# Optimization experiments

Measured on AMD Instinct MI355X. Metric: run time of the kernel, lower is better.

The kernel has to match this reference:

```python
import jax, jax.numpy as jnp
import numpy as np
from jax import lax

B, CIN, COUT, H, W = 4, 32, 64, 192, 192
K = 3  # kernel size
RED = 16  # SE reduction
EPS = 1e-5


def _conv2d_same(x, w, b):
    y = lax.conv_general_dilated(x, w, (1, 1), 'SAME',
                                 dimension_numbers=('NCHW', 'OIHW', 'NCHW'))
    return y + b[None, :, None, None]


def _bilinear_gather(x, py, px):
    # x: [B,C,H,W]; py/px: [B,KK,H,W] absolute sample coords -> [B,C,KK,H,W]
    Bb, C, Hh, Ww = x.shape
    KK = py.shape[1]
    y0 = jnp.floor(py); x0 = jnp.floor(px)
    wy = py - y0; wx = px - x0
    x_flat = x.reshape(Bb, C, Hh * Ww)

    def corner(yi, xi, wgt):
        valid = (yi >= 0) & (yi < Hh) & (xi >= 0) & (xi < Ww)
        yc = jnp.clip(yi, 0, Hh - 1).astype(jnp.int32)
        xc = jnp.clip(xi, 0, Ww - 1).astype(jnp.int32)
        idx = (yc * Ww + xc).reshape(Bb, 1, KK * Hh * Ww)
        g = jnp.take_along_axis(x_flat, idx, axis=2).reshape(Bb, C, KK, Hh, Ww)
        w_eff = (wgt * valid.astype(x.dtype))[:, None]  # [B,1,KK,H,W]
        return g * w_eff

    out = (corner(y0, x0, (1 - wy) * (1 - wx))
           + corner(y0, x0 + 1, (1 - wy) * wx)
           + corner(y0 + 1, x0, wy * (1 - wx))
           + corner(y0 + 1, x0 + 1, wy * wx))
    return out  # [B,C,KK,H,W]


def _deform_conv(x, offsets, w, b):
    # torchvision DeformConv2d, stride 1, pad 1, dilation 1, 1 offset group.
    Bb, C, Hh, Ww = x.shape
    off = offsets.reshape(Bb, K * K, 2, Hh, Ww)
    dy, dx = off[:, :, 0], off[:, :, 1]  # [B,KK,H,W]
    ky, kx = jnp.meshgrid(jnp.arange(K) - 1, jnp.arange(K) - 1, indexing='ij')
    hg, wg = jnp.meshgrid(jnp.arange(Hh), jnp.arange(Ww), indexing='ij')
    py = hg[None, None] + ky.reshape(-1)[None, :, None, None] + dy
    px = wg[None, None] + kx.reshape(-1)[None, :, None, None] + dx
    sampled = _bilinear_gather(x, py, px)  # [B,CIN,KK,H,W]
    y = jnp.einsum('bckhw,ock->bohw', sampled, w.reshape(w.shape[0], C, K * K))
    return y + b[None, :, None, None]


def _forward(x, w_off, b_off, w_def, b_def, bn_gamma, bn_beta,
             fc1_w, fc1_b, fc2_w, fc2_b):
    offsets = _conv2d_same(x, w_off, b_off)
    y = _deform_conv(x, offsets, w_def, b_def)
    # BatchNorm2d (training-mode batch statistics)
    mean = jnp.mean(y, axis=(0, 2, 3), keepdims=True)
    var = jnp.var(y, axis=(0, 2, 3), keepdims=True)
    y = (y - mean) * lax.rsqrt(var + EPS)
    y = y * bn_gamma[None, :, None, None] + bn_beta[None, :, None, None]
    # SE layer
    s = jnp.mean(y, axis=(2, 3))  # [B,C]
    s = jax.nn.relu(s @ fc1_w.T + fc1_b)
    s = jax.nn.sigmoid(s @ fc2_w.T + fc2_b)
    y = y * s[:, :, None, None]
    y = jax.nn.relu(y)
    # MaxPool 2x2 stride 2
    y = lax.reduce_window(y, -jnp.inf, lax.max, (1, 1, 2, 2), (1, 1, 2, 2), 'VALID')
    return y


def setup_inputs() -> dict:
    key = jax.random.key(0)
    ks = jax.random.split(key, 12)
    rn = lambda k, s, sc=1.0: (jax.random.normal(k, s, dtype=jnp.float32) * sc)
    return {
        'x': rn(ks[0], (B, CIN, H, W)),
        'w_off': rn(ks[1], (2 * K * K, CIN, K, K), 0.02),
        'b_off': jnp.zeros((2 * K * K,), jnp.float32),
        'w_def': rn(ks[2], (COUT, CIN, K, K), 0.05),
        'b_def': rn(ks[3], (COUT,), 0.05),
        'bn_gamma': jnp.ones((COUT,), jnp.float32),
        'bn_beta': jnp.zeros((COUT,), jnp.float32),
        'fc1_w': rn(ks[4], (COUT // RED, COUT), 0.1),
        'fc1_b': jnp.zeros((COUT // RED,), jnp.float32),
        'fc2_w': rn(ks[5], (COUT, COUT // RED), 0.1),
        'fc2_b': jnp.zeros((COUT,), jnp.float32),
    }


def reference(x, w_off, b_off, w_def, b_def, bn_gamma, bn_beta,
              fc1_w, fc1_b, fc2_w, fc2_b):
    return _forward(x, w_off, b_off, w_def, b_def, bn_gamma, bn_beta,
                    fc1_w, fc1_b, fc2_w, fc2_b)
```

## Files before the change

### kernel.cpp

```cpp
#include <hip/hip_runtime.h>
#include <math.h>

#define B_    4
#define CIN_  32
#define COUT_ 64
#define H_    192
#define W_    192
#define HW_   (H_ * W_)
#define NPIX_ (B_ * HW_)
#define EPS_  1e-5f

static __device__ __forceinline__ int swz1152(int blk) {
    return ((blk & 7) * 144) + (blk >> 3);
}
static __device__ __forceinline__ int swz2304(int blk) {
    return ((blk & 7) * 288) + (blk >> 3);
}

struct Cr { int o00, o01, o10, o11; float w00, w01, w10, w11; };

__global__ __launch_bounds__(256) void k_pre(
    const float* __restrict__ x, const float* __restrict__ w_def,
    const float* __restrict__ w_off, float* __restrict__ xt,
    float* __restrict__ wt_def, float* __restrict__ wt_off,
    float* __restrict__ stats)
{
    if (blockIdx.x < NPIX_ / 256) {
        const int pid = blockIdx.x * 256 + threadIdx.x;
        const int b   = pid / HW_;
        const int rem = pid - b * HW_;
        const float* xb = x + (size_t)b * CIN_ * HW_ + rem;
        float4 v[8];
#pragma unroll
        for (int j = 0; j < 8; ++j) {
            v[j].x = xb[(j * 4 + 0) * HW_];
            v[j].y = xb[(j * 4 + 1) * HW_];
            v[j].z = xb[(j * 4 + 2) * HW_];
            v[j].w = xb[(j * 4 + 3) * HW_];
        }
        float4* dst = (float4*)(xt + (size_t)pid * 32);
#pragma unroll
        for (int j = 0; j < 8; ++j) dst[j] = v[j];
    } else {
        const int i = (blockIdx.x - NPIX_ / 256) * 256 + threadIdx.x;
        if (i < 18432) {
            const int o  = i & 63;
            const int c  = (i >> 6) & 31;
            const int kk = i >> 11;
            wt_def[i] = w_def[(o * 32 + c) * 9 + kk];
        } else if (i < 18432 + 5760) {
            const int e  = i - 18432;
            const int c  = e & 31;
            const int t  = e >> 5;
            const int o  = t % 20;
            const int kk = t / 20;
            wt_off[e] = (o < 18) ? w_off[(o * 32 + c) * 9 + kk] : 0.f;
        } else if (i < 18432 + 5760 + 512) {
            stats[i - 18432 - 5760] = 0.f;
        }
    }
}

__global__ __launch_bounds__(256, 6) void k_conv_off(
    const float* __restrict__ xt, const float* __restrict__ wt,
    const float* __restrict__ b_off, float* __restrict__ offs)
{
    __shared__ float4 tile[8][198];
    const int tid = threadIdx.x;
    const int px  = tid & 63;
    const int og  = __builtin_amdgcn_readfirstlane(tid >> 6);

    const int blk  = swz2304(blockIdx.x);
    const int base = blk * 64;
    const int b    = base / HW_;
    const int rem0 = base - b * HW_;
    const int h0   = rem0 / W_;
    const int w0   = rem0 - h0 * W_;

    const float* xb = xt + (size_t)b * HW_ * 32;
    for (int i = tid; i < 1584; i += 256) {
        const int j   = i & 7;
        const int rec = i >> 3;
        const int r   = rec / 66;
        const int cc  = rec - r * 66;
        const int hc  = min(max(h0 + r - 1, 0), H_ - 1);
        const int wc  = min(max(w0 + cc - 1, 0), W_ - 1);
        tile[j][rec] = *(const float4*)(xb + (hc * W_ + wc) * 32 + j * 4);
    }
    __syncthreads();

    const bool rv0 = (h0 - 1 >= 0), rv2 = (h0 + 1 < H_);
    float acc[5] = {0.f, 0.f, 0.f, 0.f, 0.f};

#pragma unroll 1
    for (int kk = 0; kk < 9; ++kk) {
        const int ky = kk / 3, kx = kk % 3;
        const bool rok = (ky == 0) ? rv0 : ((ky == 2) ? rv2 : true);
        const int wcol = w0 + px + kx - 1;
        const float g = (rok && wcol >= 0 && wcol < W_) ? 1.f : 0.f;
        const int rec = ky * 66 + px + kx;

        float4 v[8];
#pragma unroll
        for (int j = 0; j < 8; ++j) {
            v[j] = tile[j][rec];
            v[j].x *= g; v[j].y *= g; v[j].z *= g; v[j].w *= g;
        }
        const float* wk = wt + (kk * 20 + og * 5) * 32;
#pragma unroll
        for (int oo = 0; oo < 5; ++oo) {
            const float4* wr = (const float4*)(wk + oo * 32);
            float s = acc[oo];
#pragma unroll
            for (int j = 0; j < 8; ++j) {
                const float4 wv = wr[j];
                s += v[j].x * wv.x + v[j].y * wv.y
                   + v[j].z * wv.z + v[j].w * wv.w;
            }
            acc[oo] = s;
        }
    }

    const int rem = rem0 + px;
#pragma unroll
    for (int oo = 0; oo < 5; ++oo) {
        const int o = og * 5 + oo;
        if (o < 18)
            offs[(b * 18 + o) * HW_ + rem] = acc[oo] + b_off[o];
    }
}

__global__ __launch_bounds__(512, 6) void k_deform(
    const float* __restrict__ xt, const float* __restrict__ offs,
    const float* __restrict__ wt, const float* __restrict__ b_def,
    float* __restrict__ y, float* __restrict__ sum_bc,
    float* __restrict__ sumsq_bc)
{
    __shared__ float vlds[32 * 128];
    const int tid  = threadIdx.x;
    const int px   = tid & 127;
    const int grp  = __builtin_amdgcn_readfirstlane(tid >> 7);
    const int lane = tid & 63;
    const int pid  = swz1152(blockIdx.x) * 128 + px;
    const int b    = pid / HW_;
    const int rem  = pid - b * HW_;
    const int h    = rem / W_;
    const int w    = rem - h * W_;
    const float* xg = xt + (size_t)b * HW_ * 32 + grp * 8;
    const float* ob = offs + b * 18 * HW_ + rem;

    float acc[16];
#pragma unroll
    for (int q = 0; q < 16; ++q) acc[q] = 0.f;

    auto mk = [&](int kk, float dy, float dx) -> Cr {
        const float py = (float)(h + kk / 3 - 1) + dy;
        const float qx = (float)(w + kk % 3 - 1) + dx;
        const float y0f = floorf(py), x0f = floorf(qx);
        const float wy = py - y0f, wx = qx - x0f;
        const int iy0 = (int)y0f, ix0 = (int)x0f;
        const int iy1 = iy0 + 1,  ix1 = ix0 + 1;
        const float vy0 = (iy0 >= 0 && iy0 < H_) ? 1.f : 0.f;
        const float vy1 = (iy1 >= 0 && iy1 < H_) ? 1.f : 0.f;
        const float vx0 = (ix0 >= 0 && ix0 < W_) ? 1.f : 0.f;
        const float vx1 = (ix1 >= 0 && ix1 < W_) ? 1.f : 0.f;
        Cr c;
        c.w00 = (1.f - wy) * (1.f - wx) * vy0 * vx0;
        c.w01 = (1.f - wy) * wx * vy0 * vx1;
        c.w10 = wy * (1.f - wx) * vy1 * vx0;
        c.w11 = wy * wx * vy1 * vx1;
        const int cy0 = min(max(iy0, 0), H_ - 1), cy1 = min(max(iy1, 0), H_ - 1);
        const int cx0 = min(max(ix0, 0), W_ - 1), cx1 = min(max(ix1, 0), W_ - 1);
        c.o00 = (cy0 * W_ + cx0) * 32; c.o01 = (cy0 * W_ + cx1) * 32;
        c.o10 = (cy1 * W_ + cx0) * 32; c.o11 = (cy1 * W_ + cx1) * 32;
        return c;
    };

    float dy = ob[0], dx = ob[HW_];
    Cr cur = mk(0, dy, dx);
    float4 A0 = *(const float4*)(xg + cur.o00), A1 = *(const float4*)(xg + cur.o00 + 4);
    float4 B0 = *(const float4*)(xg + cur.o01), B1 = *(const float4*)(xg + cur.o01 + 4);
    float4 C0 = *(const float4*)(xg + cur.o10), C1 = *(const float4*)(xg + cur.o10 + 4);
    float4 D0 = *(const float4*)(xg + cur.o11), D1 = *(const float4*)(xg + cur.o11 + 4);
    float ndy = ob[2 * HW_], ndx = ob[3 * HW_];

#pragma unroll 1
    for (int kk = 0; kk < 9; ++kk) {
        __syncthreads();
        float v[8];
        v[0] = cur.w00 * A0.x + cur.w01 * B0.x + cur.w10 * C0.x + cur.w11 * D0.x;
        v[1] = cur.w00 * A0.y + cur.w01 * B0.y + cur.w10 * C0.y + cur.w11 * D0.y;
        v[2] = cur.w00 * A0.z + cur.w01 * B0.z + cur.w10 * C0.z + cur.w11 * D0.z;
        v[3] = cur.w00 * A0.w + cur.w01 * B0.w + cur.w10 * C0.w + cur.w11 * D0.w;
        v[4] = cur.w00 * A1.x + cur.w01 * B1.x + cur.w10 * C1.x + cur.w11 * D1.x;
        v[5] = cur.w00 * A1.y + cur.w01 * B1.y + cur.w10 * C1.y + cur.w11 * D1.y;
        v[6] = cur.w00 * A1.z + cur.w01 * B1.z + cur.w10 * C1.z + cur.w11 * D1.z;
        v[7] = cur.w00 * A1.w + cur.w01 * B1.w + cur.w10 * C1.w + cur.w11 * D1.w;
#pragma unroll
        for (int j = 0; j < 8; ++j) vlds[(grp * 8 + j) * 128 + px] = v[j];

        if (kk < 8) {
            cur = mk(kk + 1, ndy, ndx);
            A0 = *(const float4*)(xg + cur.o00); A1 = *(const float4*)(xg + cur.o00 + 4);
            B0 = *(const float4*)(xg + cur.o01); B1 = *(const float4*)(xg + cur.o01 + 4);
            C0 = *(const float4*)(xg + cur.o10); C1 = *(const float4*)(xg + cur.o10 + 4);
            D0 = *(const float4*)(xg + cur.o11); D1 = *(const float4*)(xg + cur.o11 + 4);
            if (kk < 7) {
                ndy = ob[(2 * kk + 4) * HW_];
                ndx = ob[(2 * kk + 5) * HW_];
            }
        }
        __syncthreads();

        const float* wk = wt + (kk << 11) + (grp << 4);
#pragma unroll 8
        for (int c = 0; c < 32; ++c) {
            const float vv = vlds[c * 128 + px];
            const float4* wr = (const float4*)(wk + (c << 6));
            const float4 w0 = wr[0], w1 = wr[1], w2 = wr[2], w3 = wr[3];
            acc[ 0] += vv * w0.x; acc[ 1] += vv * w0.y;
            acc[ 2] += vv * w0.z; acc[ 3] += vv * w0.w;
            acc[ 4] += vv * w1.x; acc[ 5] += vv * w1.y;
            acc[ 6] += vv * w1.z; acc[ 7] += vv * w1.w;
            acc[ 8] += vv * w2.x; acc[ 9] += vv * w2.y;
            acc[10] += vv * w2.z; acc[11] += vv * w2.w;
            acc[12] += vv * w3.x; acc[13] += vv * w3.y;
            acc[14] += vv * w3.z; acc[15] += vv * w3.w;
        }
    }

    float* yp = y + ((size_t)b * COUT_ + grp * 16) * HW_ + rem;
#pragma unroll
    for (int q = 0; q < 16; ++q) {
        acc[q] += b_def[grp * 16 + q];
        yp[q * HW_] = acc[q];
    }

    float ls = 0.f, lq = 0.f;
#pragma unroll
    for (int o = 0; o < 16; ++o) {
        float t = acc[o];
        float u = t * t;
#pragma unroll
        for (int s = 32; s; s >>= 1) {
            t += __shfl_xor(t, s, 64);
            u += __shfl_xor(u, s, 64);
        }
        if (lane == o) { ls = t; lq = u; }
    }
    if (lane < 16) {
        atomicAdd(&sum_bc[b * 64 + grp * 16 + lane], ls);
        atomicAdd(&sumsq_bc[b * 64 + grp * 16 + lane], lq);
    }
}

__global__ __launch_bounds__(256) void k_finish(
    const float* __restrict__ y,
    const float* __restrict__ sum_bc, const float* __restrict__ sumsq_bc,
    const float* __restrict__ gamma, const float* __restrict__ beta,
    const float* __restrict__ fc1_w, const float* __restrict__ fc1_b,
    const float* __restrict__ fc2_w, const float* __restrict__ fc2_b,
    float* __restrict__ out)
{
    __shared__ float sal[256], sbb[256], sin_[256];
    const int tid = threadIdx.x;
    {
        const int b = tid >> 6, c = tid & 63;
        float ch_s = 0.f, ch_q = 0.f;
#pragma unroll
        for (int bb = 0; bb < 4; ++bb) {
            ch_s += sum_bc[bb * 64 + c];
            ch_q += sumsq_bc[bb * 64 + c];
        }
        const float invN = 1.f / (float)(B_ * HW_);
        const float mean = ch_s * invN;
        const float var  = ch_q * invN - mean * mean;
        const float a    = gamma[c] * rsqrtf(var + EPS_);
        const float bi   = beta[c] - mean * a;
        sin_[tid] = a * (sum_bc[tid] * (1.f / (float)HW_)) + bi;
        __syncthreads();
        float hv[4];
#pragma unroll
        for (int j = 0; j < 4; ++j) {
            float hs = fc1_b[j];
            for (int cc = 0; cc < 64; ++cc)
                hs += sin_[b * 64 + cc] * fc1_w[j * 64 + cc];
            hv[j] = fmaxf(hs, 0.f);
        }
        float o = fc2_b[c];
#pragma unroll
        for (int j = 0; j < 4; ++j) o += hv[j] * fc2_w[c * 4 + j];
        const float s = 1.f / (1.f + expf(-o));
        sal[tid] = a * s;
        sbb[tid] = bi * s;
    }
    __syncthreads();

    const int t    = blockIdx.x * 256 + tid;
    const int opix = t * 2;
    const int bc   = opix / (96 * 96);
    const int rem  = opix - bc * (96 * 96);
    const int oh   = rem / 96, ow = rem - oh * 96;
    const float al = sal[bc], bb = sbb[bc];
    const float* yp = y + (size_t)bc * HW_ + (2 * oh) * W_ + 2 * ow;
    const float4 r0 = *(const float4*)yp;
    const float4 r1 = *(const float4*)(yp + W_);
    float2 st;
    st.x = fmaxf(fmaxf(fmaxf(fmaf(r0.x, al, bb), fmaf(r0.y, al, bb)),
                       fmaxf(fmaf(r1.x, al, bb), fmaf(r1.y, al, bb))), 0.f);
    st.y = fmaxf(fmaxf(fmaxf(fmaf(r0.z, al, bb), fmaf(r0.w, al, bb)),
                       fmaxf(fmaf(r1.z, al, bb), fmaf(r1.w, al, bb))), 0.f);
    *(float2*)(out + opix) = st;
}

extern "C" void kernel_launch(void* const* d_in, const int* in_sizes, int n_in,
                              void* d_out, int out_size, void* d_ws, size_t ws_size,
                              hipStream_t stream)
{
    const float* x     = (const float*)d_in[0];
    const float* w_off = (const float*)d_in[1];
    const float* b_off = (const float*)d_in[2];
    const float* w_def = (const float*)d_in[3];
    const float* b_def = (const float*)d_in[4];
    const float* gamma = (const float*)d_in[5];
    const float* beta  = (const float*)d_in[6];
    const float* fc1_w = (const float*)d_in[7];
    const float* fc1_b = (const float*)d_in[8];
    const float* fc2_w = (const float*)d_in[9];
    const float* fc2_b = (const float*)d_in[10];
    float* out = (float*)d_out;

    float* ws   = (float*)d_ws;
    float* offs   = ws;
    float* yb     = offs + 2654208;
    float* xt     = yb + 9437184;
    float* wt_def = xt + 4718592;
    float* wt_off = wt_def + 18432;
    float* stats  = wt_off + 5760;
    float* sum_bc   = stats;
    float* sumsq_bc = stats + 256;

    k_pre     <<<dim3(NPIX_ / 256 + 97), dim3(256), 0, stream>>>(
                  x, w_def, w_off, xt, wt_def, wt_off, stats);
    k_conv_off<<<dim3(NPIX_ / 64), dim3(256), 0, stream>>>(xt, wt_off, b_off, offs);
    k_deform  <<<dim3(NPIX_ / 128), dim3(512), 0, stream>>>(xt, offs, wt_def, b_def,
                                                            yb, sum_bc, sumsq_bc);
    k_finish  <<<dim3(B_ * COUT_ * 96 * 96 / 512), dim3(256), 0, stream>>>(
                  yb, sum_bc, sumsq_bc, gamma, beta,
                  fc1_w, fc1_b, fc2_w, fc2_b, out);
}
```

Before: 264.7 us.

## Fuse offset conv into deformable conv kernel with LDS double-buffered sampling

Merges the offset-prediction convolution and the deformable convolution into one kernel. Offsets now stay in shared memory and are never written to or read back from global memory. The block shrinks from 128 to 64 pixels with 4 groups of 16 output channels each. The per-tap sampled values are double-buffered in LDS, so each tap needs one barrier instead of two and the next tap's gathers overlap the current FMA loop. The trade-off is one fewer kernel launch and less offset traffic, against smaller blocks, reuse of the tile buffer, and possible register pressure from holding the prefetched corners across the inner loop.

Measured after the change: 224.6 us. 15.1% less time.

```diff
diff --git a/kernel.cpp b/kernel.cpp
--- a/kernel.cpp
+++ b/kernel.cpp
@@ -10,9 +10,6 @@
 #define NPIX_ (B_ * HW_)
 #define EPS_  1e-5f
 
-static __device__ __forceinline__ int swz1152(int blk) {
-    return ((blk & 7) * 144) + (blk >> 3);
-}
 static __device__ __forceinline__ int swz2304(int blk) {
     return ((blk & 7) * 288) + (blk >> 3);
 }
@@ -61,14 +58,21 @@
     }
 }
 
-__global__ __launch_bounds__(256, 6) void k_conv_off(
-    const float* __restrict__ xt, const float* __restrict__ wt,
-    const float* __restrict__ b_off, float* __restrict__ offs)
+__global__ __launch_bounds__(256, 6) void k_fused(
+    const float* __restrict__ xt, const float* __restrict__ wto,
+    const float* __restrict__ b_off, const float* __restrict__ wtd,
+    const float* __restrict__ b_def, float* __restrict__ y,
+    float* __restrict__ sum_bc, float* __restrict__ sumsq_bc)
 {
-    __shared__ float4 tile[8][198];
-    const int tid = threadIdx.x;
-    const int px  = tid & 63;
-    const int og  = __builtin_amdgcn_readfirstlane(tid >> 6);
+    __shared__ __align__(16) float smem[6336];
+    __shared__ float offlds[20 * 64];
+    float4 (*tile)[198] = (float4(*)[198])smem;
+    float* vbuf = smem;
+
+    const int tid  = threadIdx.x;
+    const int px   = tid & 63;
+    const int og   = __builtin_amdgcn_readfirstlane(tid >> 6);
+    const int lane = tid & 63;
 
     const int blk  = swz2304(blockIdx.x);
     const int base = blk * 64;
@@ -76,8 +80,8 @@
     const int rem0 = base - b * HW_;
     const int h0   = rem0 / W_;
     const int w0   = rem0 - h0 * W_;
-
     const float* xb = xt + (size_t)b * HW_ * 32;
+
     for (int i = tid; i < 1584; i += 256) {
         const int j   = i & 7;
         const int rec = i >> 3;
@@ -89,71 +93,56 @@
     }
     __syncthreads();
 
-    const bool rv0 = (h0 - 1 >= 0), rv2 = (h0 + 1 < H_);
-    float acc[5] = {0.f, 0.f, 0.f, 0.f, 0.f};
-
+    {
+        const bool rv0 = (h0 - 1 >= 0), rv2 = (h0 + 1 < H_);
+        float acc5[5] = {0.f, 0.f, 0.f, 0.f, 0.f};
 #pragma unroll 1
-    for (int kk = 0; kk < 9; ++kk) {
-        const int ky = kk / 3, kx = kk % 3;
-        const bool rok = (ky == 0) ? rv0 : ((ky == 2) ? rv2 : true);
-        const int wcol = w0 + px + kx - 1;
-        const float g = (rok && wcol >= 0 && wcol < W_) ? 1.f : 0.f;
-        const int rec = ky * 66 + px + kx;
-
-        float4 v[8];
-#pragma unroll
-        for (int j = 0; j < 8; ++j) {
-            v[j] = tile[j][rec];
-            v[j].x *= g; v[j].y *= g; v[j].z *= g; v[j].w *= g;
-        }
-        const float* wk = wt + (kk * 20 + og * 5) * 32;
+        for (int kk = 0; kk < 9; ++kk) {
+            const int ky = kk / 3, kx = kk % 3;
+            const bool rok = (ky == 0) ? rv0 : ((ky == 2) ? rv2 : true);
+            const int wcol = w0 + px + kx - 1;
+            const float g = (rok && wcol >= 0 && wcol < W_) ? 1.f : 0.f;
+            const int rec = ky * 66 + px + kx;
+
+            float4 v[8];
+#pragma unroll
+            for (int j = 0; j < 8; ++j) {
+                v[j] = tile[j][rec];
+                v[j].x *= g; v[j].y *= g; v[j].z *= g; v[j].w *= g;
+            }
+            const float* wk = wto + (kk * 20 + og * 5) * 32;
+#pragma unroll
+            for (int oo = 0; oo < 5; ++oo) {
+                const float4* wr = (const float4*)(wk + oo * 32);
+                float s = acc5[oo];
+#pragma unroll
+                for (int j = 0; j < 8; ++j) {
+                    const float4 wv = wr[j];
+                    s += v[j].x * wv.x + v[j].y * wv.y
+                       + v[j].z * wv.z + v[j].w * wv.w;
+                }
+                acc5[oo] = s;
+            }
+        }
 #pragma unroll
         for (int oo = 0; oo < 5; ++oo) {
-            const float4* wr = (const float4*)(wk + oo * 32);
-            float s = acc[oo];
-#pragma unroll
-            for (int j = 0; j < 8; ++j) {
-                const float4 wv = wr[j];
-                s += v[j].x * wv.x + v[j].y * wv.y
-                   + v[j].z * wv.z + v[j].w * wv.w;
-            }
-            acc[oo] = s;
-        }
-    }
-
-    const int rem = rem0 + px;
-#pragma unroll
-    for (int oo = 0; oo < 5; ++oo) {
-        const int o = og * 5 + oo;
-        if (o < 18)
-            offs[(b * 18 + o) * HW_ + rem] = acc[oo] + b_off[o];
-    }
-}
-
-__global__ __launch_bounds__(512, 6) void k_deform(
-    const float* __restrict__ xt, const float* __restrict__ offs,
-    const float* __restrict__ wt, const float* __restrict__ b_def,
-    float* __restrict__ y, float* __restrict__ sum_bc,
-    float* __restrict__ sumsq_bc)
-{
-    __shared__ float vlds[32 * 128];
-    const int tid  = threadIdx.x;
-    const int px   = tid & 127;
-    const int grp  = __builtin_amdgcn_readfirstlane(tid >> 7);
-    const int lane = tid & 63;
-    const int pid  = swz1152(blockIdx.x) * 128 + px;
-    const int b    = pid / HW_;
-    const int rem  = pid - b * HW_;
-    const int h    = rem / W_;
-    const int w    = rem - h * W_;
-    const float* xg = xt + (size_t)b * HW_ * 32 + grp * 8;
-    const float* ob = offs + b * 18 * HW_ + rem;
+            const int o = og * 5 + oo;
+            if (o < 18) offlds[o * 64 + px] = acc5[oo] + b_off[o];
+        }
+    }
+    __syncthreads();
+
+    const int h = h0;
+    const int w = w0 + px;
+    const float* xg = xb + og * 8;
 
     float acc[16];
 #pragma unroll
     for (int q = 0; q < 16; ++q) acc[q] = 0.f;
 
-    auto mk = [&](int kk, float dy, float dx) -> Cr {
+    auto mk = [&](int kk) -> Cr {
+        const float dy = offlds[(2 * kk) * 64 + px];
+        const float dx = offlds[(2 * kk + 1) * 64 + px];
         const float py = (float)(h + kk / 3 - 1) + dy;
         const float qx = (float)(w + kk % 3 - 1) + dx;
         const float y0f = floorf(py), x0f = floorf(qx);
@@ -176,46 +165,42 @@
         return c;
     };
 
-    float dy = ob[0], dx = ob[HW_];
-    Cr cur = mk(0, dy, dx);
-    float4 A0 = *(const float4*)(xg + cur.o00), A1 = *(const float4*)(xg + cur.o00 + 4);
-    float4 B0 = *(const float4*)(xg + cur.o01), B1 = *(const float4*)(xg + cur.o01 + 4);
-    float4 C0 = *(const float4*)(xg + cur.o10), C1 = *(const float4*)(xg + cur.o10 + 4);
-    float4 D0 = *(const float4*)(xg + cur.o11), D1 = *(const float4*)(xg + cur.o11 + 4);
-    float ndy = ob[2 * HW_], ndx = ob[3 * HW_];
+    {
+        Cr c0 = mk(0);
+        float4 A0 = *(const float4*)(xg + c0.o00), A1 = *(const float4*)(xg + c0.o00 + 4);
+        float4 B0 = *(const float4*)(xg + c0.o01), B1 = *(const float4*)(xg + c0.o01 + 4);
+        float4 C0 = *(const float4*)(xg + c0.o10), C1 = *(const float4*)(xg + c0.o10 + 4);
+        float4 D0 = *(const float4*)(xg + c0.o11), D1 = *(const float4*)(xg + c0.o11 + 4);
+        float v[8];
+        v[0] = c0.w00 * A0.x + c0.w01 * B0.x + c0.w10 * C0.x + c0.w11 * D0.x;
+        v[1] = c0.w00 * A0.y + c0.w01 * B0.y + c0.w10 * C0.y + c0.w11 * D0.y;
+        v[2] = c0.w00 * A0.z + c0.w01 * B0.z + c0.w10 * C0.z + c0.w11 * D0.z;
+        v[3] = c0.w00 * A0.w + c0.w01 * B0.w + c0.w10 * C0.w + c0.w11 * D0.w;
+        v[4] = c0.w00 * A1.x + c0.w01 * B1.x + c0.w10 * C1.x + c0.w11 * D1.x;
+        v[5] = c0.w00 * A1.y + c0.w01 * B1.y + c0.w10 * C1.y + c0.w11 * D1.y;
+        v[6] = c0.w00 * A1.z + c0.w01 * B1.z + c0.w10 * C1.z + c0.w11 * D1.z;
+        v[7] = c0.w00 * A1.w + c0.w01 * B1.w + c0.w10 * C1.w + c0.w11 * D1.w;
+#pragma unroll
+        for (int j = 0; j < 8; ++j) vbuf[(og * 8 + j) * 64 + px] = v[j];
+    }
+    __syncthreads();
 
 #pragma unroll 1
     for (int kk = 0; kk < 9; ++kk) {
-        __syncthreads();
-        float v[8];
-        v[0] = cur.w00 * A0.x + cur.w01 * B0.x + cur.w10 * C0.x + cur.w11 * D0.x;
-        v[1] = cur.w00 * A0.y + cur.w01 * B0.y + cur.w10 * C0.y + cur.w11 * D0.y;
-        v[2] = cur.w00 * A0.z + cur.w01 * B0.z + cur.w10 * C0.z + cur.w11 * D0.z;
-        v[3] = cur.w00 * A0.w + cur.w01 * B0.w + cur.w10 * C0.w + cur.w11 * D0.w;
-        v[4] = cur.w00 * A1.x + cur.w01 * B1.x + cur.w10 * C1.x + cur.w11 * D1.x;
-        v[5] = cur.w00 * A1.y + cur.w01 * B1.y + cur.w10 * C1.y + cur.w11 * D1.y;
-        v[6] = cur.w00 * A1.z + cur.w01 * B1.z + cur.w10 * C1.z + cur.w11 * D1.z;
-        v[7] = cur.w00 * A1.w + cur.w01 * B1.w + cur.w10 * C1.w + cur.w11 * D1.w;
-#pragma unroll
-        for (int j = 0; j < 8; ++j) vlds[(grp * 8 + j) * 128 + px] = v[j];
-
+        Cr nx; float4 A0, A1, B0, B1, C0, C1, D0, D1;
         if (kk < 8) {
-            cur = mk(kk + 1, ndy, ndx);
-            A0 = *(const float4*)(xg + cur.o00); A1 = *(const float4*)(xg + cur.o00 + 4);
-            B0 = *(const float4*)(xg + cur.o01); B1 = *(const float4*)(xg + cur.o01 + 4);
-            C0 = *(const float4*)(xg + cur.o10); C1 = *(const float4*)(xg + cur.o10 + 4);
-            D0 = *(const float4*)(xg + cur.o11); D1 = *(const float4*)(xg + cur.o11 + 4);
-            if (kk < 7) {
-                ndy = ob[(2 * kk + 4) * HW_];
-                ndx = ob[(2 * kk + 5) * HW_];
-            }
-        }
-        __syncthreads();
-
-        const float* wk = wt + (kk << 11) + (grp << 4);
+            nx = mk(kk + 1);
+            A0 = *(const float4*)(xg + nx.o00); A1 = *(const float4*)(xg + nx.o00 + 4);
+            B0 = *(const float4*)(xg + nx.o01); B1 = *(const float4*)(xg + nx.o01 + 4);
+            C0 = *(const float4*)(xg + nx.o10); C1 = *(const float4*)(xg + nx.o10 + 4);
+            D0 = *(const float4*)(xg + nx.o11); D1 = *(const float4*)(xg + nx.o11 + 4);
+        }
+
+        const float* vp = vbuf + (kk & 1) * 2048;
+        const float* wk = wtd + (kk << 11) + (og << 4);
 #pragma unroll 8
         for (int c = 0; c < 32; ++c) {
-            const float vv = vlds[c * 128 + px];
+            const float vv = vp[c * 64 + px];
             const float4* wr = (const float4*)(wk + (c << 6));
             const float4 w0 = wr[0], w1 = wr[1], w2 = wr[2], w3 = wr[3];
             acc[ 0] += vv * w0.x; acc[ 1] += vv * w0.y;
@@ -227,12 +212,29 @@
             acc[12] += vv * w3.x; acc[13] += vv * w3.y;
             acc[14] += vv * w3.z; acc[15] += vv * w3.w;
         }
-    }
-
-    float* yp = y + ((size_t)b * COUT_ + grp * 16) * HW_ + rem;
+
+        if (kk < 8) {
+            float v[8];
+            v[0] = nx.w00 * A0.x + nx.w01 * B0.x + nx.w10 * C0.x + nx.w11 * D0.x;
+            v[1] = nx.w00 * A0.y + nx.w01 * B0.y + nx.w10 * C0.y + nx.w11 * D0.y;
+            v[2] = nx.w00 * A0.z + nx.w01 * B0.z + nx.w10 * C0.z + nx.w11 * D0.z;
+            v[3] = nx.w00 * A0.w + nx.w01 * B0.w + nx.w10 * C0.w + nx.w11 * D0.w;
+            v[4] = nx.w00 * A1.x + nx.w01 * B1.x + nx.w10 * C1.x + nx.w11 * D1.x;
+            v[5] = nx.w00 * A1.y + nx.w01 * B1.y + nx.w10 * C1.y + nx.w11 * D1.y;
+            v[6] = nx.w00 * A1.z + nx.w01 * B1.z + nx.w10 * C1.z + nx.w11 * D1.z;
+            v[7] = nx.w00 * A1.w + nx.w01 * B1.w + nx.w10 * C1.w + nx.w11 * D1.w;
+            float* wp = vbuf + ((kk + 1) & 1) * 2048;
+#pragma unroll
+            for (int j = 0; j < 8; ++j) wp[(og * 8 + j) * 64 + px] = v[j];
+            __syncthreads();
+        }
+    }
+
+    const int rem = rem0 + px;
+    float* yp = y + ((size_t)b * COUT_ + og * 16) * HW_ + rem;
 #pragma unroll
     for (int q = 0; q < 16; ++q) {
-        acc[q] += b_def[grp * 16 + q];
+        acc[q] += b_def[og * 16 + q];
         yp[q * HW_] = acc[q];
     }
 
@@ -249,8 +251,8 @@
         if (lane == o) { ls = t; lq = u; }
     }
     if (lane < 16) {
-        atomicAdd(&sum_bc[b * 64 + grp * 16 + lane], ls);
-        atomicAdd(&sumsq_bc[b * 64 + grp * 16 + lane], lq);
+        atomicAdd(&sum_bc[b * 64 + og * 16 + lane], ls);
+        atomicAdd(&sumsq_bc[b * 64 + og * 16 + lane], lq);
     }
 }
 
@@ -331,8 +333,7 @@
     float* out = (float*)d_out;
 
     float* ws   = (float*)d_ws;
-    float* offs   = ws;
-    float* yb     = offs + 2654208;
+    float* yb     = ws;
     float* xt     = yb + 9437184;
     float* wt_def = xt + 4718592;
     float* wt_off = wt_def + 18432;
@@ -340,12 +341,11 @@
     float* sum_bc   = stats;
     float* sumsq_bc = stats + 256;
 
-    k_pre     <<<dim3(NPIX_ / 256 + 97), dim3(256), 0, stream>>>(
-                  x, w_def, w_off, xt, wt_def, wt_off, stats);
-    k_conv_off<<<dim3(NPIX_ / 64), dim3(256), 0, stream>>>(xt, wt_off, b_off, offs);
-    k_deform  <<<dim3(NPIX_ / 128), dim3(512), 0, stream>>>(xt, offs, wt_def, b_def,
-                                                            yb, sum_bc, sumsq_bc);
-    k_finish  <<<dim3(B_ * COUT_ * 96 * 96 / 512), dim3(256), 0, stream>>>(
-                  yb, sum_bc, sumsq_bc, gamma, beta,
-                  fc1_w, fc1_b, fc2_w, fc2_b, out);
-}
+    k_pre   <<<dim3(NPIX_ / 256 + 97), dim3(256), 0, stream>>>(
+                x, w_def, w_off, xt, wt_def, wt_off, stats);
+    k_fused <<<dim3(NPIX_ / 64), dim3(256), 0, stream>>>(
+                xt, wt_off, b_off, wt_def, b_def, yb, sum_bc, sumsq_bc);
+    k_finish<<<dim3(B_ * COUT_ * 96 * 96 / 512), dim3(256), 0, stream>>>(
+                yb, sum_bc, sumsq_bc, gamma, beta,
+                fc1_w, fc1_b, fc2_w, fc2_b, out);
+}
```
